# Optimization experiments

Hardware: AMD Instinct MI355X
Metric: run time of the kernel (lower is better)

The kernel has to match this reference:

```python
import jax, jax.numpy as jnp
import numpy as np

HID = 128
N_LAYERS = 4


def setup_inputs() -> dict:
    key = jax.random.key(0)
    ks = jax.random.split(key, 16)
    B, T, N, F = 64, 168, 64, 17
    x = jax.random.normal(ks[0], (B, T, N, F), dtype=jnp.float32)
    adj = jax.random.randint(ks[1], (N, N), 0, 2, dtype=jnp.int32)
    s = 0.05
    W1 = jax.random.normal(ks[2], (F, HID), dtype=jnp.float32) * s
    a1 = jax.random.normal(ks[3], (2 * HID,), dtype=jnp.float32) * s
    W2 = jax.random.normal(ks[4], (HID, HID), dtype=jnp.float32) * s
    a2 = jax.random.normal(ks[5], (2 * HID,), dtype=jnp.float32) * s
    # PyTorch LSTM weights, 4 layers, gate order i,f,g,o; layer0 input=HID
    Wih = jax.random.normal(ks[6], (N_LAYERS, 4 * HID, HID), dtype=jnp.float32) * s
    Whh = jax.random.normal(ks[7], (N_LAYERS, 4 * HID, HID), dtype=jnp.float32) * s
    bih = jax.random.normal(ks[8], (N_LAYERS, 4 * HID), dtype=jnp.float32) * s
    bhh = jax.random.normal(ks[9], (N_LAYERS, 4 * HID), dtype=jnp.float32) * s
    Wlin = jax.random.normal(ks[10], (1, N_LAYERS * HID), dtype=jnp.float32) * s
    blin = jax.random.normal(ks[11], (1,), dtype=jnp.float32) * s
    return {"x": x, "adj": adj, "W1": W1, "a1": a1, "W2": W2, "a2": a2,
            "Wih": Wih, "Whh": Whh, "bih": bih, "bhh": bhh,
            "Wlin": Wlin, "blin": blin, "site_idx": 10}


def _gat(x, W, a, adj_mask):
    # x: [B,T,N,F] -> h: [B,T,N,O]; dense adjacency-masked attention
    h = jnp.einsum('btnf,fo->btno', x, W)
    O = W.shape[1]
    src = h @ a[:O]          # [B,T,N]  a^T[Wh_i || .]
    dst = h @ a[O:]          # [B,T,N]  a^T[. || Wh_j]
    e = jax.nn.leaky_relu(src[..., :, None] + dst[..., None, :], 0.2)  # [B,T,N,N]
    e = jnp.where(adj_mask, e, jnp.float32(-1e9))
    attn = jax.nn.softmax(e, axis=-1)
    return jnp.einsum('btij,btjo->btio', attn, h)


def _lstm_layer(x_seq, Wih_l, Whh_l, b_l):
    # x_seq: [B,T,H]; PyTorch gate order i,f,g,o
    B = x_seq.shape[0]
    h0 = jnp.zeros((B, HID), x_seq.dtype)

    def step(carry, x_t):
        h, c = carry
        g = x_t @ Wih_l.T + h @ Whh_l.T + b_l
        i, f, gg, o = jnp.split(g, 4, axis=-1)
        c = jax.nn.sigmoid(f) * c + jax.nn.sigmoid(i) * jnp.tanh(gg)
        h = jax.nn.sigmoid(o) * jnp.tanh(c)
        return (h, c), h

    (hT, cT), ys = jax.lax.scan(step, (h0, h0), jnp.swapaxes(x_seq, 0, 1))
    return jnp.swapaxes(ys, 0, 1), hT


def reference(x, adj, W1, a1, W2, a2, Wih, Whh, bih, bhh, Wlin, blin, site_idx):
    N = adj.shape[0]
    adj_mask = (adj > 0) | jnp.eye(N, dtype=bool)  # self-loops avoid empty rows
    h = _gat(x, W1, a1, adj_mask)
    h = _gat(h, W2, a2, adj_mask)
    seq = h[:, :, site_idx, :]                     # [B,T,HID]
    h_finals = []
    for l in range(N_LAYERS):
        seq, hT = _lstm_layer(seq, Wih[l], Whh[l], bih[l] + bhh[l])
        h_finals.append(hT)
    hcat = jnp.concatenate(h_finals, axis=-1)      # [B, 4*HID] == permute+reshape
    out = hcat @ Wlin.T + blin                     # [B,1]
    return out.squeeze(-1)
```

## Files before the change

### kernel.cpp

```cpp
#include <hip/hip_runtime.h>
#include <hip/hip_bf16.h>

#define BB 64
#define TT 168
#define NN 64
#define FF 17
#define HID 128
#define GATES 512
#define NLAYERS 4
#define NROWS (BB*TT)

#define CH 8
#define NCHUNK (TT/CH)

#define WS_W1SRC 0
#define WS_W1DST 32
#define WS_W2SRC 64
#define WS_W2DST 192
#define WS_BSUM  320
#define WS_WD    2560
#define WS_WSV   2592
#define WS_W12   2624
#define WS_WXG0T 4800
#define WS_ADJB  15104
#define WS_FLAGS 16000
#define WS_XG    1395712
#define WS_HSEQ0 6900736
#define HSEQ_SZ  1376256

__device__ __forceinline__ void lds_barrier() {
    __asm__ volatile("" ::: "memory");
    __builtin_amdgcn_s_waitcnt(0xc07f);
    __builtin_amdgcn_s_barrier();
    __asm__ volatile("" ::: "memory");
}

__device__ __forceinline__ float fsig(float x) {
    return __builtin_amdgcn_rcpf(1.f + __expf(-x));
}
__device__ __forceinline__ float ftanh(float x) {
    float e = __expf(2.f * x);
    return 1.f - 2.f * __builtin_amdgcn_rcpf(e + 1.f);
}
__device__ __forceinline__ float bcast_lane(float v, int lane) {
    return __int_as_float(__builtin_amdgcn_readlane(__float_as_int(v), lane));
}

__global__ void prep1(const float* __restrict__ W1, const float* __restrict__ a1,
                      const float* __restrict__ W2, const float* __restrict__ a2,
                      const float* __restrict__ bih, const float* __restrict__ bhh,
                      const int* __restrict__ adj, float* __restrict__ ws) {
    int tid = threadIdx.x;
    if (tid < 34) {
        int f = tid % FF, half = tid / FF;
        float acc = 0.f;
        for (int o = 0; o < HID; o++) acc += W1[f*HID + o] * a1[half*HID + o];
        ws[(half ? WS_W1DST : WS_W1SRC) + f] = acc;
    }
    {
        int k = tid & 127, half = tid >> 7;
        float acc = 0.f;
        for (int o = 0; o < HID; o++) acc += W2[k*HID + o] * a2[half*HID + o];
        ws[(half ? WS_W2DST : WS_W2SRC) + k] = acc;
    }
    for (int idx = tid; idx < NLAYERS*GATES; idx += 256) ws[WS_BSUM + idx] = bih[idx] + bhh[idx];
    if (tid < 64) {
        unsigned long long m = 1ull << tid;
        const int* ar = adj + tid*64;
        for (int j = 0; j < 64; j++) if (ar[j] > 0) m |= (1ull << j);
        ((unsigned long long*)(ws + WS_ADJB))[tid] = m;
    }
    __hip_atomic_store((int*)(ws + WS_FLAGS) + tid, 0,
                       __ATOMIC_RELAXED, __HIP_MEMORY_SCOPE_AGENT);
}

__global__ void prep2(const float* __restrict__ W1, const float* __restrict__ W2,
                      float* __restrict__ ws) {
    int f = blockIdx.x, o = threadIdx.x;
    float acc = 0.f;
    for (int k = 0; k < HID; k++) acc += W1[f*HID + k] * W2[k*HID + o];
    ws[WS_W12 + f*HID + o] = acc;
}

__global__ void prep3(const float* __restrict__ W1, const float* __restrict__ Wih0,
                      float* __restrict__ ws) {
    int idx = blockIdx.x * 256 + threadIdx.x;
    if (idx < 17) {
        int f = idx;
        float acc = 0.f;
        for (int k = 0; k < HID; k++) acc += W1[f*HID + k] * ws[WS_W2DST + k];
        ws[WS_WD + f] = acc;
    } else if (idx < 34) {
        int f = idx - 17;
        float acc = 0.f;
        for (int k = 0; k < HID; k++) acc += W1[f*HID + k] * ws[WS_W2SRC + k];
        ws[WS_WSV + f] = acc;
    } else if (idx < 34 + GATES*FF) {
        int e = idx - 34;
        int j = e % GATES, f = e / GATES;
        float acc = 0.f;
        for (int o = 0; o < HID; o++) acc += ws[WS_W12 + f*HID + o] * Wih0[j*HID + o];
        ws[WS_WXG0T + j*20 + f] = acc;
    }
}

struct __align__(16) GatSmem {
    float attn[64*68];
    float xsT[FF*64];
    float xbarT[FF*68];
    float src1[64], dst1[64], rinv[64], att2[64];
    float xbar2[20];
    float part_x[FF*8];
    unsigned long long adjbits[64];
};

__global__ __launch_bounds__(256) void gat_fused(const float* __restrict__ x, const int* __restrict__ adj,
                                                 const float* __restrict__ ws,
                                                 float* __restrict__ Xg, const int* __restrict__ site_ptr) {
    __shared__ GatSmem sm;
    const int tid = threadIdx.x;
    const int tt = blockIdx.x, bb = blockIdx.y;
    const int site = site_ptr[0];
    const int r = bb*TT + tt;
    const float* xblk = x + (size_t)r * (NN*FF);

    for (int idx = tid; idx < NN*FF; idx += 256) {
        int n = idx / FF, f = idx % FF;
        sm.xsT[f*64 + n] = xblk[idx];
    }
    if (tid < 64) sm.adjbits[tid] = ((const unsigned long long*)(ws + WS_ADJB))[tid];
    lds_barrier();

    if (tid < 128) {
        int n = tid & 63, half = tid >> 6;
        const float* wv = ws + (half ? WS_W1DST : WS_W1SRC);
        float acc = 0.f;
        #pragma unroll
        for (int f = 0; f < FF; f++) acc += sm.xsT[f*64 + n] * wv[f];
        if (half) sm.dst1[n] = acc; else sm.src1[n] = acc;
    }
    lds_barrier();

    {
        int q = tid & 3, i = tid >> 2;
        unsigned long long ab = sm.adjbits[i];
        float si = sm.src1[i];
        float v[16];
        float vmax = -1e30f;
        #pragma unroll
        for (int u = 0; u < 16; u++) {
            int jj = q*16 + u;
            float e = si + sm.dst1[jj];
            float lv = fmaxf(e, 0.2f*e);
            lv = ((ab >> jj) & 1ull) ? lv : -1e9f;
            v[u] = lv;
            vmax = fmaxf(vmax, lv);
        }
        vmax = fmaxf(vmax, __shfl_xor(vmax, 1, 4));
        vmax = fmaxf(vmax, __shfl_xor(vmax, 2, 4));
        float s = 0.f;
        float* arow = &sm.attn[i*68];
        #pragma unroll
        for (int w = 0; w < 4; w++) {
            float4 pv;
            pv.x = __expf(v[w*4+0] - vmax);
            pv.y = __expf(v[w*4+1] - vmax);
            pv.z = __expf(v[w*4+2] - vmax);
            pv.w = __expf(v[w*4+3] - vmax);
            s += (pv.x + pv.y) + (pv.z + pv.w);
            *(float4*)(arow + q*16 + w*4) = pv;
        }
        s += __shfl_xor(s, 1, 4);
        s += __shfl_xor(s, 2, 4);
        if (q == 0) sm.rinv[i] = 1.f / s;
    }
    lds_barrier();

    {
        int i = tid & 63, q = tid >> 6;
        const float* arow = &sm.attn[i*68];
        float acc[5] = {0.f,0.f,0.f,0.f,0.f};
        const int nf = (q == 0) ? 5 : 4;
        for (int j4 = 0; j4 < 16; j4++) {
            float4 a4 = *(const float4*)(arow + j4*4);
            #pragma unroll
            for (int u = 0; u < 5; u++) {
                if (u < nf) {
                    int f = q + 4*u;
                    float4 x4 = *(const float4*)(&sm.xsT[f*64 + j4*4]);
                    acc[u] += a4.x*x4.x + a4.y*x4.y + a4.z*x4.z + a4.w*x4.w;
                }
            }
        }
        float ri = sm.rinv[i];
        #pragma unroll
        for (int u = 0; u < 5; u++) {
            if (u < nf) sm.xbarT[(q + 4*u)*68 + i] = acc[u] * ri;
        }
    }
    lds_barrier();

    if (tid < 64) {
        int jj = tid;
        float d = 0.f, sp = 0.f;
        #pragma unroll
        for (int f = 0; f < FF; f++) {
            float xv = sm.xbarT[f*68 + jj];
            float xs = sm.xbarT[f*68 + site];
            d  += xv * ws[WS_WD + f];
            sp += xs * ws[WS_WSV + f];
        }
        unsigned long long ab = sm.adjbits[site];
        float e = sp + d;
        float lv = fmaxf(e, 0.2f*e);
        lv = ((ab >> jj) & 1ull) ? lv : -1e9f;
        float m = lv;
        #pragma unroll
        for (int dd = 1; dd < 64; dd <<= 1) m = fmaxf(m, __shfl_xor(m, dd));
        float p = __expf(lv - m);
        float s = p;
        #pragma unroll
        for (int dd = 1; dd < 64; dd <<= 1) s += __shfl_xor(s, dd);
        sm.att2[jj] = p / s;
    }
    lds_barrier();

    if (tid < FF*8) {
        int f = tid >> 3, c = tid & 7;
        float p = 0.f;
        #pragma unroll
        for (int u = 0; u < 8; u++) {
            int i = c*8 + u;
            p += sm.att2[i] * sm.xbarT[f*68 + i];
        }
        sm.part_x[f*8 + c] = p;
    }
    lds_barrier();

    if (tid < FF) {
        float s = 0.f;
        #pragma unroll
        for (int c = 0; c < 8; c++) s += sm.part_x[tid*8 + c];
        sm.xbar2[tid] = s;
    }
    lds_barrier();

    {
        float xb[FF];
        #pragma unroll
        for (int f = 0; f < FF; f++) xb[f] = sm.xbar2[f];
        #pragma unroll
        for (int half = 0; half < 2; half++) {
            int j = tid + half*256;
            const float4* wp = (const float4*)(ws + WS_WXG0T + j*20);
            float4 w0 = wp[0], w1 = wp[1], w2 = wp[2], w3 = wp[3];
            float wlast = ws[WS_WXG0T + j*20 + 16];
            float acc = ws[WS_BSUM + j];
            acc += w0.x*xb[0] + w0.y*xb[1] + w0.z*xb[2] + w0.w*xb[3];
            acc += w1.x*xb[4] + w1.y*xb[5] + w1.z*xb[6] + w1.w*xb[7];
            acc += w2.x*xb[8] + w2.y*xb[9] + w2.z*xb[10] + w2.w*xb[11];
            acc += w3.x*xb[12] + w3.y*xb[13] + w3.z*xb[14] + w3.w*xb[15];
            acc += wlast*xb[16];
            Xg[(size_t)r*GATES + j] = acc;
        }
    }
}

__global__ __launch_bounds__(512)
__attribute__((amdgpu_waves_per_eu(2, 2)))
void lstm_pipe(const float* __restrict__ Xg0,
               const float* __restrict__ Wih,
               const float* __restrict__ Whh,
               float* __restrict__ ws) {
    const int b = blockIdx.x;
    const int l = blockIdx.y;
    const int tid = threadIdx.x;
    const int lane = tid & 63;
    const int kc = tid >> 7;
    const int jj = tid & 127;
    const int o = kc*32 + (lane & 31);
    const bool blane = (lane < 32);
    const bool storer = ((tid >> 6) & 1) == 0;

    __shared__ __align__(16) float part[2][4][128][4];
    __shared__ __align__(16) float xg[2][CH*GATES];
    __shared__ __align__(16) float xs[2][CH*HID];
    __shared__ __align__(16) float lds_pad[6656];

    int* flags = (int*)(ws + WS_FLAGS);

    if (__hip_atomic_load(&flags[255], __ATOMIC_RELAXED, __HIP_MEMORY_SCOPE_AGENT) == 0x7fffffff) {
        lds_pad[tid] = (float)tid;
        __builtin_amdgcn_s_waitcnt(0xc07f);
        ((float*)ws)[tid] = lds_pad[tid ^ 1];
    }

    float w[4][32];
    {
        const float* Whh_l = Whh + (size_t)l*GATES*HID;
        #pragma unroll
        for (int u = 0; u < 4; u++) {
            const float4* wr2 = (const float4*)(Whh_l + (size_t)(u*128 + jj)*HID + kc*32);
            #pragma unroll
            for (int k4 = 0; k4 < 8; k4++) {
                float4 v4 = wr2[k4];
                w[u][k4*4+0] = v4.x; w[u][k4*4+1] = v4.y; w[u][k4*4+2] = v4.z; w[u][k4*4+3] = v4.w;
            }
        }
    }

    const float* xg_g  = Xg0 + (size_t)b*TT*GATES;
    float*       hout  = ws + WS_HSEQ0 + (size_t)l*HSEQ_SZ + (size_t)b*TT*HID;
    const float* hprev = (l > 0) ? (ws + WS_HSEQ0 + (size_t)(l-1)*HSEQ_SZ + (size_t)b*TT*HID)
                                 : ws;
    const float* Wih_l = Wih + (size_t)l*GATES*HID;
    const float  bsum_j = ws[WS_BSUM + l*GATES + tid];
    const float4* wr = (const float4*)(Wih_l + (size_t)tid*HID);

    float h_own = 0.f, c_own = 0.f;
    float4 pf0 = {0,0,0,0}, pf1 = {0,0,0,0};
    int buf = 0;

    float acc[CH];
    float4 wv0, wv1, wv2, wv3;

    if (l == 0) {
        const float4* g4 = (const float4*)xg_g;
        float4 v0 = g4[tid], v1 = g4[512 + tid];
        float4* d = (float4*)xg[0];
        d[tid] = v0; d[512 + tid] = v1;
        lds_barrier();
    } else {
        if (tid == 0) {
            int* flg = &flags[(l-1)*BB + b];
            while (__hip_atomic_load(flg, __ATOMIC_RELAXED, __HIP_MEMORY_SCOPE_AGENT) < CH)
                __builtin_amdgcn_s_sleep(8);
        }
        lds_barrier();
        #pragma unroll
        for (int q = 0; q < 2; q++) {
            int idx = q*512 + tid;
            xs[0][idx] = __hip_atomic_load(&hprev[idx],
                                           __ATOMIC_RELAXED, __HIP_MEMORY_SCOPE_AGENT);
        }
        lds_barrier();
        float a0[CH];
        #pragma unroll
        for (int t = 0; t < CH; t++) a0[t] = bsum_j;
        #pragma unroll
        for (int kq = 0; kq < 4; kq++) {
            float4 wvv[8];
            #pragma unroll
            for (int q = 0; q < 8; q++) wvv[q] = wr[kq*8 + q];
            #pragma unroll
            for (int t = 0; t < CH; t++) {
                const float4* xp = (const float4*)(&xs[0][t*HID + kq*32]);
                float a = 0.f;
                #pragma unroll
                for (int q = 0; q < 8; q++) {
                    float4 xv = xp[q];
                    a += wvv[q].x*xv.x + wvv[q].y*xv.y + wvv[q].z*xv.z + wvv[q].w*xv.w;
                }
                a0[t] += a;
            }
        }
        #pragma unroll
        for (int t = 0; t < CH; t++) xg[0][t*GATES + tid] = a0[t];
        wv0 = wr[0]; wv1 = wr[1]; wv2 = wr[2]; wv3 = wr[3];
        #pragma unroll
        for (int t = 0; t < CH; t++) acc[t] = bsum_j;
        lds_barrier();
    }

    for (int c = 0; c < NCHUNK; c++) {
        const bool have_next = (c + 1 < NCHUNK);

        if (l == 0) {
            if (have_next) {
                const float4* g4 = (const float4*)(xg_g + (size_t)(c+1)*CH*GATES);
                pf0 = g4[tid]; pf1 = g4[512 + tid];
            }
        } else if (have_next) {
            if (tid == 0) {
                int* flg = &flags[(l-1)*BB + b];
                const int need = (c + 2)*CH;
                while (__hip_atomic_load(flg, __ATOMIC_RELAXED, __HIP_MEMORY_SCOPE_AGENT) < need)
                    __builtin_amdgcn_s_sleep(8);
            }
            lds_barrier();
            float v0 = __hip_atomic_load(&hprev[(size_t)(c+1)*CH*HID + tid],
                                         __ATOMIC_RELAXED, __HIP_MEMORY_SCOPE_AGENT);
            float v1 = __hip_atomic_load(&hprev[(size_t)(c+1)*CH*HID + 512 + tid],
                                         __ATOMIC_RELAXED, __HIP_MEMORY_SCOPE_AGENT);
            xs[(c+1)&1][tid] = v0;
            xs[(c+1)&1][512 + tid] = v1;
        }

        const float* xgbuf = (l == 0) ? xg[buf] : xg[c & 1];
        const float* xsn = xs[(c+1)&1];
        float* xgn = xg[(c+1)&1];

        for (int tc = 0; tc < CH; tc++) {
            const int t = c*CH + tc;
            float xgc[4];
            if (blane) {
                #pragma unroll
                for (int u = 0; u < 4; u++) xgc[u] = xgbuf[tc*GATES + u*HID + o];
            }
            float a0 = 0.f, a1 = 0.f, a2 = 0.f, a3 = 0.f;
            #pragma unroll
            for (int k = 0; k < 32; k++) {
                float hv = bcast_lane(h_own, k);
                a0 += w[0][k]*hv; a1 += w[1][k]*hv; a2 += w[2][k]*hv; a3 += w[3][k]*hv;
            }
            float4 st = {a0, a1, a2, a3};
            *(float4*)(&part[t & 1][kc][jj][0]) = st;

            lds_barrier();

            if (l > 0 && have_next) {
                const int kb = tc*16;
                #pragma unroll
                for (int t2 = 0; t2 < CH; t2++) {
                    const float4* xp = (const float4*)(&xsn[t2*HID + kb]);
                    float4 x0 = xp[0], x1 = xp[1], x2 = xp[2], x3 = xp[3];
                    acc[t2] += wv0.x*x0.x + wv0.y*x0.y + wv0.z*x0.z + wv0.w*x0.w
                             + wv1.x*x1.x + wv1.y*x1.y + wv1.z*x1.z + wv1.w*x1.w
                             + wv2.x*x2.x + wv2.y*x2.y + wv2.z*x2.z + wv2.w*x2.w
                             + wv3.x*x3.x + wv3.y*x3.y + wv3.z*x3.z + wv3.w*x3.w;
                }
                const int ns = (tc + 1) & 7;
                wv0 = wr[ns*4+0]; wv1 = wr[ns*4+1]; wv2 = wr[ns*4+2]; wv3 = wr[ns*4+3];
                if (tc == CH-1) {
                    #pragma unroll
                    for (int t2 = 0; t2 < CH; t2++) {
                        xgn[t2*GATES + tid] = acc[t2];
                        acc[t2] = bsum_j;
                    }
                }
            }

            if (blane) {
                float4 s4 = {xgc[0], xgc[1], xgc[2], xgc[3]};
                #pragma unroll
                for (int kcc = 0; kcc < 4; kcc++) {
                    float4 p = *(const float4*)(&part[t & 1][kcc][o][0]);
                    s4.x += p.x; s4.y += p.y; s4.z += p.z; s4.w += p.w;
                }
                float si = fsig(s4.x), sf = fsig(s4.y), so = fsig(s4.w);
                float tg = ftanh(s4.z);
                c_own = sf*c_own + si*tg;
                h_own = so*ftanh(c_own);
                if (storer)
                    __hip_atomic_store(&hout[t*HID + o], h_own,
                                       __ATOMIC_RELAXED, __HIP_MEMORY_SCOPE_AGENT);
            }
        }

        if (l == 0) {
            __asm__ volatile("s_waitcnt vmcnt(0)" ::: "memory");
            if (have_next) {
                float4* d = (float4*)xg[buf ^ 1];
                d[tid] = pf0; d[512 + tid] = pf1;
                buf ^= 1;
            }
            lds_barrier();
            if (tid == 0)
                __hip_atomic_store(&flags[b], (c+1)*CH,
                                   __ATOMIC_RELAXED, __HIP_MEMORY_SCOPE_AGENT);
        } else {
            __asm__ volatile("s_waitcnt vmcnt(0)" ::: "memory");
            lds_barrier();
            if (l < NLAYERS - 1 && tid == 0)
                __hip_atomic_store(&flags[l*BB + b], (c+1)*CH,
                                   __ATOMIC_RELAXED, __HIP_MEMORY_SCOPE_AGENT);
        }
    }
}

__global__ void final_lin(const float* __restrict__ ws, const float* __restrict__ Wlin,
                          const float* __restrict__ blin, float* __restrict__ out) {
    const int b = blockIdx.x, l = threadIdx.x;
    float acc = 0.f;
    #pragma unroll
    for (int u = 0; u < 8; u++) {
        int idx = u*64 + l;
        int layer = idx >> 7, k = idx & 127;
        const float* hs = ws + WS_HSEQ0 + (size_t)layer*HSEQ_SZ;
        acc += hs[((size_t)b*TT + (TT-1))*HID + k] * Wlin[idx];
    }
    #pragma unroll
    for (int d = 1; d < 64; d <<= 1) acc += __shfl_xor(acc, d);
    if (l == 0) out[b] = acc + blin[0];
}

extern "C" void kernel_launch(void* const* d_in, const int* in_sizes, int n_in,
                              void* d_out, int out_size, void* d_ws, size_t ws_size,
                              hipStream_t stream) {
    const float* x    = (const float*)d_in[0];
    const int*   adj  = (const int*)d_in[1];
    const float* W1   = (const float*)d_in[2];
    const float* a1   = (const float*)d_in[3];
    const float* W2   = (const float*)d_in[4];
    const float* a2   = (const float*)d_in[5];
    const float* Wih  = (const float*)d_in[6];
    const float* Whh  = (const float*)d_in[7];
    const float* bih  = (const float*)d_in[8];
    const float* bhh  = (const float*)d_in[9];
    const float* Wlin = (const float*)d_in[10];
    const float* blin = (const float*)d_in[11];
    const int*   site = (const int*)d_in[12];
    float* ws  = (float*)d_ws;
    float* out = (float*)d_out;

    prep1<<<1, 256, 0, stream>>>(W1, a1, W2, a2, bih, bhh, adj, ws);
    prep2<<<FF, 128, 0, stream>>>(W1, W2, ws);
    prep3<<<35, 256, 0, stream>>>(W1, Wih, ws);
    gat_fused<<<dim3(TT, BB), 256, 0, stream>>>(x, adj, ws, ws + WS_XG, site);
    lstm_pipe<<<dim3(BB, NLAYERS), 512, 0, stream>>>(ws + WS_XG, Wih, Whh, ws);
    final_lin<<<64, 64, 0, stream>>>(ws, Wlin, blin, out);
}
```

Measured before the change: 613.3 us.

## Halve LSTM block to 256 threads and broadcast hidden state via LDS

The LSTM recurrence block shrinks from 512 to 256 threads. Each thread now holds a 64-wide slice of four Whh rows and two Wih rows. The per-step hidden-state broadcast moves from readlane shuffles of a register to float4 reads from a double-buffered LDS hbuf. The K-split partial sums drop from four to two. This cuts the cross-wave reduction and readlane serialization per timestep, but adds a second barrier per step and doubles the input-projection work per thread.

After: 753.2 us. +22.8%, slower.

```diff
diff --git a/kernel.cpp b/kernel.cpp
--- a/kernel.cpp
+++ b/kernel.cpp
@@ -41,9 +41,6 @@
 __device__ __forceinline__ float ftanh(float x) {
     float e = __expf(2.f * x);
     return 1.f - 2.f * __builtin_amdgcn_rcpf(e + 1.f);
-}
-__device__ __forceinline__ float bcast_lane(float v, int lane) {
-    return __int_as_float(__builtin_amdgcn_readlane(__float_as_int(v), lane));
 }
 
 __global__ void prep1(const float* __restrict__ W1, const float* __restrict__ a1,
@@ -266,8 +263,8 @@
     }
 }
 
-__global__ __launch_bounds__(512)
-__attribute__((amdgpu_waves_per_eu(2, 2)))
+__global__ __launch_bounds__(256)
+__attribute__((amdgpu_waves_per_eu(1, 1)))
 void lstm_pipe(const float* __restrict__ Xg0,
                const float* __restrict__ Wih,
                const float* __restrict__ Whh,
@@ -276,16 +273,16 @@
     const int l = blockIdx.y;
     const int tid = threadIdx.x;
     const int lane = tid & 63;
-    const int kc = tid >> 7;
+    const int kc2 = tid >> 7;
     const int jj = tid & 127;
-    const int o = kc*32 + (lane & 31);
+    const int o = (tid >> 6)*32 + (lane & 31);
     const bool blane = (lane < 32);
-    const bool storer = ((tid >> 6) & 1) == 0;
-
-    __shared__ __align__(16) float part[2][4][128][4];
+
+    __shared__ __align__(16) float part[2][2][128][4];
     __shared__ __align__(16) float xg[2][CH*GATES];
     __shared__ __align__(16) float xs[2][CH*HID];
-    __shared__ __align__(16) float lds_pad[6656];
+    __shared__ __align__(16) float hbuf[2][HID];
+    __shared__ __align__(16) float lds_pad[9216];
 
     int* flags = (int*)(ws + WS_FLAGS);
 
@@ -295,17 +292,14 @@
         ((float*)ws)[tid] = lds_pad[tid ^ 1];
     }
 
-    float w[4][32];
+    float4 w4[4][16];
     {
         const float* Whh_l = Whh + (size_t)l*GATES*HID;
         #pragma unroll
         for (int u = 0; u < 4; u++) {
-            const float4* wr2 = (const float4*)(Whh_l + (size_t)(u*128 + jj)*HID + kc*32);
+            const float4* p = (const float4*)(Whh_l + (size_t)(u*128 + jj)*HID + kc2*64);
             #pragma unroll
-            for (int k4 = 0; k4 < 8; k4++) {
-                float4 v4 = wr2[k4];
-                w[u][k4*4+0] = v4.x; w[u][k4*4+1] = v4.y; w[u][k4*4+2] = v4.z; w[u][k4*4+3] = v4.w;
-            }
+            for (int k4 = 0; k4 < 16; k4++) w4[u][k4] = p[k4];
         }
     }
 
@@ -314,21 +308,26 @@
     const float* hprev = (l > 0) ? (ws + WS_HSEQ0 + (size_t)(l-1)*HSEQ_SZ + (size_t)b*TT*HID)
                                  : ws;
     const float* Wih_l = Wih + (size_t)l*GATES*HID;
-    const float  bsum_j = ws[WS_BSUM + l*GATES + tid];
-    const float4* wr = (const float4*)(Wih_l + (size_t)tid*HID);
+    const float  bsA = ws[WS_BSUM + l*GATES + tid];
+    const float  bsB = ws[WS_BSUM + l*GATES + 256 + tid];
+    const float4* wrA = (const float4*)(Wih_l + (size_t)tid*HID);
+    const float4* wrB = (const float4*)(Wih_l + (size_t)(256 + tid)*HID);
 
     float h_own = 0.f, c_own = 0.f;
-    float4 pf0 = {0,0,0,0}, pf1 = {0,0,0,0};
+    float4 pf0 = {0,0,0,0}, pf1 = {0,0,0,0}, pf2 = {0,0,0,0}, pf3 = {0,0,0,0};
     int buf = 0;
 
-    float acc[CH];
-    float4 wv0, wv1, wv2, wv3;
+    float accA[CH], accB[CH];
+    float4 wva0, wva1, wva2, wva3;
+    float4 wvb0, wvb1, wvb2, wvb3;
+
+    if (blane) hbuf[0][o] = 0.f;
 
     if (l == 0) {
         const float4* g4 = (const float4*)xg_g;
-        float4 v0 = g4[tid], v1 = g4[512 + tid];
         float4* d = (float4*)xg[0];
-        d[tid] = v0; d[512 + tid] = v1;
+        #pragma unroll
+        for (int q = 0; q < 4; q++) d[q*256 + tid] = g4[q*256 + tid];
         lds_barrier();
     } else {
         if (tid == 0) {
@@ -338,37 +337,41 @@
         }
         lds_barrier();
         #pragma unroll
-        for (int q = 0; q < 2; q++) {
-            int idx = q*512 + tid;
+        for (int q = 0; q < 4; q++) {
+            int idx = q*256 + tid;
             xs[0][idx] = __hip_atomic_load(&hprev[idx],
                                            __ATOMIC_RELAXED, __HIP_MEMORY_SCOPE_AGENT);
         }
         lds_barrier();
-        float a0[CH];
-        #pragma unroll
-        for (int t = 0; t < CH; t++) a0[t] = bsum_j;
-        #pragma unroll
-        for (int kq = 0; kq < 4; kq++) {
-            float4 wvv[8];
+        float aA[CH], aB[CH];
+        #pragma unroll
+        for (int t = 0; t < CH; t++) { aA[t] = bsA; aB[t] = bsB; }
+        for (int s = 0; s < CH; s++) {
+            float4 qa0 = wrA[s*4+0], qa1 = wrA[s*4+1], qa2 = wrA[s*4+2], qa3 = wrA[s*4+3];
+            float4 qb0 = wrB[s*4+0], qb1 = wrB[s*4+1], qb2 = wrB[s*4+2], qb3 = wrB[s*4+3];
             #pragma unroll
-            for (int q = 0; q < 8; q++) wvv[q] = wr[kq*8 + q];
-            #pragma unroll
-            for (int t = 0; t < CH; t++) {
-                const float4* xp = (const float4*)(&xs[0][t*HID + kq*32]);
-                float a = 0.f;
-                #pragma unroll
-                for (int q = 0; q < 8; q++) {
-                    float4 xv = xp[q];
-                    a += wvv[q].x*xv.x + wvv[q].y*xv.y + wvv[q].z*xv.z + wvv[q].w*xv.w;
-                }
-                a0[t] += a;
-            }
-        }
-        #pragma unroll
-        for (int t = 0; t < CH; t++) xg[0][t*GATES + tid] = a0[t];
-        wv0 = wr[0]; wv1 = wr[1]; wv2 = wr[2]; wv3 = wr[3];
-        #pragma unroll
-        for (int t = 0; t < CH; t++) acc[t] = bsum_j;
+            for (int t2 = 0; t2 < CH; t2++) {
+                const float4* xp = (const float4*)(&xs[0][t2*HID + s*16]);
+                float4 x0 = xp[0], x1 = xp[1], x2 = xp[2], x3 = xp[3];
+                aA[t2] += qa0.x*x0.x + qa0.y*x0.y + qa0.z*x0.z + qa0.w*x0.w
+                        + qa1.x*x1.x + qa1.y*x1.y + qa1.z*x1.z + qa1.w*x1.w
+                        + qa2.x*x2.x + qa2.y*x2.y + qa2.z*x2.z + qa2.w*x2.w
+                        + qa3.x*x3.x + qa3.y*x3.y + qa3.z*x3.z + qa3.w*x3.w;
+                aB[t2] += qb0.x*x0.x + qb0.y*x0.y + qb0.z*x0.z + qb0.w*x0.w
+                        + qb1.x*x1.x + qb1.y*x1.y + qb1.z*x1.z + qb1.w*x1.w
+                        + qb2.x*x2.x + qb2.y*x2.y + qb2.z*x2.z + qb2.w*x2.w
+                        + qb3.x*x3.x + qb3.y*x3.y + qb3.z*x3.z + qb3.w*x3.w;
+            }
+        }
+        #pragma unroll
+        for (int t = 0; t < CH; t++) {
+            xg[0][t*GATES + tid]       = aA[t];
+            xg[0][t*GATES + 256 + tid] = aB[t];
+        }
+        wva0 = wrA[0]; wva1 = wrA[1]; wva2 = wrA[2]; wva3 = wrA[3];
+        wvb0 = wrB[0]; wvb1 = wrB[1]; wvb2 = wrB[2]; wvb3 = wrB[3];
+        #pragma unroll
+        for (int t = 0; t < CH; t++) { accA[t] = bsA; accB[t] = bsB; }
         lds_barrier();
     }
 
@@ -378,7 +381,8 @@
         if (l == 0) {
             if (have_next) {
                 const float4* g4 = (const float4*)(xg_g + (size_t)(c+1)*CH*GATES);
-                pf0 = g4[tid]; pf1 = g4[512 + tid];
+                pf0 = g4[0*256 + tid]; pf1 = g4[1*256 + tid];
+                pf2 = g4[2*256 + tid]; pf3 = g4[3*256 + tid];
             }
         } else if (have_next) {
             if (tid == 0) {
@@ -388,12 +392,12 @@
                     __builtin_amdgcn_s_sleep(8);
             }
             lds_barrier();
-            float v0 = __hip_atomic_load(&hprev[(size_t)(c+1)*CH*HID + tid],
-                                         __ATOMIC_RELAXED, __HIP_MEMORY_SCOPE_AGENT);
-            float v1 = __hip_atomic_load(&hprev[(size_t)(c+1)*CH*HID + 512 + tid],
-                                         __ATOMIC_RELAXED, __HIP_MEMORY_SCOPE_AGENT);
-            xs[(c+1)&1][tid] = v0;
-            xs[(c+1)&1][512 + tid] = v1;
+            #pragma unroll
+            for (int q = 0; q < 4; q++) {
+                int idx = q*256 + tid;
+                xs[(c+1)&1][idx] = __hip_atomic_load(&hprev[(size_t)(c+1)*CH*HID + idx],
+                                                     __ATOMIC_RELAXED, __HIP_MEMORY_SCOPE_AGENT);
+            }
         }
 
         const float* xgbuf = (l == 0) ? xg[buf] : xg[c & 1];
@@ -402,66 +406,82 @@
 
         for (int tc = 0; tc < CH; tc++) {
             const int t = c*CH + tc;
-            float xgc[4];
+            float xgc0, xgc1, xgc2, xgc3;
             if (blane) {
+                xgc0 = xgbuf[tc*GATES + 0*HID + o];
+                xgc1 = xgbuf[tc*GATES + 1*HID + o];
+                xgc2 = xgbuf[tc*GATES + 2*HID + o];
+                xgc3 = xgbuf[tc*GATES + 3*HID + o];
+            }
+            float a0 = 0.f, a1 = 0.f, a2 = 0.f, a3 = 0.f;
+            {
+                const float4* hb = (const float4*)(&hbuf[t & 1][kc2*64]);
                 #pragma unroll
-                for (int u = 0; u < 4; u++) xgc[u] = xgbuf[tc*GATES + u*HID + o];
-            }
-            float a0 = 0.f, a1 = 0.f, a2 = 0.f, a3 = 0.f;
-            #pragma unroll
-            for (int k = 0; k < 32; k++) {
-                float hv = bcast_lane(h_own, k);
-                a0 += w[0][k]*hv; a1 += w[1][k]*hv; a2 += w[2][k]*hv; a3 += w[3][k]*hv;
+                for (int k4 = 0; k4 < 16; k4++) {
+                    float4 h4 = hb[k4];
+                    a0 += w4[0][k4].x*h4.x + w4[0][k4].y*h4.y + w4[0][k4].z*h4.z + w4[0][k4].w*h4.w;
+                    a1 += w4[1][k4].x*h4.x + w4[1][k4].y*h4.y + w4[1][k4].z*h4.z + w4[1][k4].w*h4.w;
+                    a2 += w4[2][k4].x*h4.x + w4[2][k4].y*h4.y + w4[2][k4].z*h4.z + w4[2][k4].w*h4.w;
+                    a3 += w4[3][k4].x*h4.x + w4[3][k4].y*h4.y + w4[3][k4].z*h4.z + w4[3][k4].w*h4.w;
+                }
             }
             float4 st = {a0, a1, a2, a3};
-            *(float4*)(&part[t & 1][kc][jj][0]) = st;
+            *(float4*)(&part[t & 1][kc2][jj][0]) = st;
 
             lds_barrier();
 
+            if (blane) {
+                float4 p0 = *(const float4*)(&part[t & 1][0][o][0]);
+                float4 p1 = *(const float4*)(&part[t & 1][1][o][0]);
+                float gi = xgc0 + p0.x + p1.x;
+                float gf = xgc1 + p0.y + p1.y;
+                float gg = xgc2 + p0.z + p1.z;
+                float go = xgc3 + p0.w + p1.w;
+                float si = fsig(gi), sf = fsig(gf), so = fsig(go);
+                float tg = ftanh(gg);
+                c_own = sf*c_own + si*tg;
+                h_own = so*ftanh(c_own);
+                hbuf[(t + 1) & 1][o] = h_own;
+                __hip_atomic_store(&hout[t*HID + o], h_own,
+                                   __ATOMIC_RELAXED, __HIP_MEMORY_SCOPE_AGENT);
+            }
+
             if (l > 0 && have_next) {
-                const int kb = tc*16;
                 #pragma unroll
                 for (int t2 = 0; t2 < CH; t2++) {
-                    const float4* xp = (const float4*)(&xsn[t2*HID + kb]);
+                    const float4* xp = (const float4*)(&xsn[t2*HID + tc*16]);
                     float4 x0 = xp[0], x1 = xp[1], x2 = xp[2], x3 = xp[3];
-                    acc[t2] += wv0.x*x0.x + wv0.y*x0.y + wv0.z*x0.z + wv0.w*x0.w
-                             + wv1.x*x1.x + wv1.y*x1.y + wv1.z*x1.z + wv1.w*x1.w
-                             + wv2.x*x2.x + wv2.y*x2.y + wv2.z*x2.z + wv2.w*x2.w
-                             + wv3.x*x3.x + wv3.y*x3.y + wv3.z*x3.z + wv3.w*x3.w;
+                    accA[t2] += wva0.x*x0.x + wva0.y*x0.y + wva0.z*x0.z + wva0.w*x0.w
+                              + wva1.x*x1.x + wva1.y*x1.y + wva1.z*x1.z + wva1.w*x1.w
+                              + wva2.x*x2.x + wva2.y*x2.y + wva2.z*x2.z + wva2.w*x2.w
+                              + wva3.x*x3.x + wva3.y*x3.y + wva3.z*x3.z + wva3.w*x3.w;
+                    accB[t2] += wvb0.x*x0.x + wvb0.y*x0.y + wvb0.z*x0.z + wvb0.w*x0.w
+                              + wvb1.x*x1.x + wvb1.y*x1.y + wvb1.z*x1.z + wvb1.w*x1.w
+                              + wvb2.x*x2.x + wvb2.y*x2.y + wvb2.z*x2.z + wvb2.w*x2.w
+                              + wvb3.x*x3.x + wvb3.y*x3.y + wvb3.z*x3.z + wvb3.w*x3.w;
                 }
                 const int ns = (tc + 1) & 7;
-                wv0 = wr[ns*4+0]; wv1 = wr[ns*4+1]; wv2 = wr[ns*4+2]; wv3 = wr[ns*4+3];
-                if (tc == CH-1) {
+                wva0 = wrA[ns*4+0]; wva1 = wrA[ns*4+1]; wva2 = wrA[ns*4+2]; wva3 = wrA[ns*4+3];
+                wvb0 = wrB[ns*4+0]; wvb1 = wrB[ns*4+1]; wvb2 = wrB[ns*4+2]; wvb3 = wrB[ns*4+3];
+                if (tc == CH - 1) {
                     #pragma unroll
                     for (int t2 = 0; t2 < CH; t2++) {
-                        xgn[t2*GATES + tid] = acc[t2];
-                        acc[t2] = bsum_j;
+                        xgn[t2*GATES + tid]       = accA[t2];
+                        xgn[t2*GATES + 256 + tid] = accB[t2];
+                        accA[t2] = bsA; accB[t2] = bsB;
                     }
                 }
             }
 
-            if (blane) {
-                float4 s4 = {xgc[0], xgc[1], xgc[2], xgc[3]};
-                #pragma unroll
-                for (int kcc = 0; kcc < 4; kcc++) {
-                    float4 p = *(const float4*)(&part[t & 1][kcc][o][0]);
-                    s4.x += p.x; s4.y += p.y; s4.z += p.z; s4.w += p.w;
-                }
-                float si = fsig(s4.x), sf = fsig(s4.y), so = fsig(s4.w);
-                float tg = ftanh(s4.z);
-                c_own = sf*c_own + si*tg;
-                h_own = so*ftanh(c_own);
-                if (storer)
-                    __hip_atomic_store(&hout[t*HID + o], h_own,
-                                       __ATOMIC_RELAXED, __HIP_MEMORY_SCOPE_AGENT);
-            }
+            lds_barrier();
         }
 
         if (l == 0) {
             __asm__ volatile("s_waitcnt vmcnt(0)" ::: "memory");
             if (have_next) {
                 float4* d = (float4*)xg[buf ^ 1];
-                d[tid] = pf0; d[512 + tid] = pf1;
+                d[0*256 + tid] = pf0; d[1*256 + tid] = pf1;
+                d[2*256 + tid] = pf2; d[3*256 + tid] = pf3;
                 buf ^= 1;
             }
             lds_barrier();
@@ -517,6 +537,6 @@
     prep2<<<FF, 128, 0, stream>>>(W1, W2, ws);
     prep3<<<35, 256, 0, stream>>>(W1, Wih, ws);
     gat_fused<<<dim3(TT, BB), 256, 0, stream>>>(x, adj, ws, ws + WS_XG, site);
-    lstm_pipe<<<dim3(BB, NLAYERS), 512, 0, stream>>>(ws + WS_XG, Wih, Whh, ws);
+    lstm_pipe<<<dim3(BB, NLAYERS), 256, 0, stream>>>(ws + WS_XG, Wih, Whh, ws);
     final_lin<<<64, 64, 0, stream>>>(ws, Wlin, blin, out);
 }
```
